# Kernel tuning notes

Measured on AMD Instinct MI355X. Metric: run time of the kernel, lower is better.

The kernel has to match this reference:

```python
import jax, jax.numpy as jnp
import numpy as np

B, S, D, H = 4, 2048, 1024, 16
HD = D // H


def setup_inputs() -> dict:
    key = jax.random.key(0)
    ks = jax.random.split(key, 9)
    s = 1.0 / np.sqrt(D)
    return {
        "x": jax.random.normal(ks[0], (B, S, D), dtype=jnp.float32),
        "Wq": jax.random.normal(ks[1], (D, D), dtype=jnp.float32) * s,
        "bq": jnp.zeros((D,), dtype=jnp.float32),
        "Wk": jax.random.normal(ks[2], (D, D), dtype=jnp.float32) * s,
        "bk": jnp.zeros((D,), dtype=jnp.float32),
        "Wv": jax.random.normal(ks[3], (D, D), dtype=jnp.float32) * s,
        "bv": jnp.zeros((D,), dtype=jnp.float32),
        "Wo": jax.random.normal(ks[4], (D, D), dtype=jnp.float32) * s,
        "bo": jnp.zeros((D,), dtype=jnp.float32),
    }


def reference(x, Wq, bq, Wk, bk, Wv, bv, Wo, bo):
    b, s, d = x.shape
    # project and split heads -> [b, h, s, hd]
    def split_heads(t):
        return t.reshape(b, s, H, HD).transpose(0, 2, 1, 3)
    q = split_heads(x @ Wq.T + bq)
    k = split_heads(x @ Wk.T + bk)
    v = split_heads(x @ Wv.T + bv)
    scale = 1.0 / np.sqrt(HD).astype(np.float32)
    att = jnp.einsum('bhqd,bhkd->bhqk', q, k) * scale
    causal = jnp.tril(jnp.ones((s, s), dtype=bool))
    att = jnp.where(causal[None, None], att, -jnp.inf)
    att = jax.nn.softmax(att, axis=-1)
    out = jnp.einsum('bhqk,bhkd->bhqd', att, v)  # [b,h,s,hd]
    out = out.transpose(0, 2, 1, 3).reshape(b, s, d)
    return out @ Wo.T + bo
```

## Files before the change

### kernel.cpp

```cpp
#include <hip/hip_runtime.h>
#include <hip/hip_bf16.h>
#include <math.h>

typedef __hip_bfloat16 bf16;
typedef __attribute__((ext_vector_type(8))) __bf16 bf16x8;
typedef __attribute__((ext_vector_type(4))) float f32x4;

__device__ __forceinline__ void gload_lds16(const void* g, void* l) {
  __builtin_amdgcn_global_load_lds(
      (const __attribute__((address_space(1))) unsigned int*)g,
      (__attribute__((address_space(3))) unsigned int*)l, 16, 0, 0);
}

__global__ void cvt_bf16(const float* __restrict__ in, bf16* __restrict__ out, int n) {
  int idx = (blockIdx.x * blockDim.x + threadIdx.x) * 8;
  if (idx >= n) return;
  float4 v0 = *(const float4*)(in + idx);
  float4 v1 = *(const float4*)(in + idx + 4);
  alignas(16) bf16 tmp[8];
  tmp[0] = __float2bfloat16(v0.x); tmp[1] = __float2bfloat16(v0.y);
  tmp[2] = __float2bfloat16(v0.z); tmp[3] = __float2bfloat16(v0.w);
  tmp[4] = __float2bfloat16(v1.x); tmp[5] = __float2bfloat16(v1.y);
  tmp[6] = __float2bfloat16(v1.z); tmp[7] = __float2bfloat16(v1.w);
  *(uint4*)(out + idx) = *(const uint4*)tmp;
}

__global__ void prep_w(const float* __restrict__ Wq, const float* __restrict__ Wk,
                       const float* __restrict__ Wv, const float* __restrict__ Wo,
                       const float* __restrict__ bq, const float* __restrict__ bk,
                       const float* __restrict__ bv,
                       bf16* __restrict__ wqkv, bf16* __restrict__ wo16,
                       float* __restrict__ b3) {
  const int bi = blockIdx.x;
  if (bi < 2048) {
    const int seg = bi >> 9;
    const int idx = ((bi & 511) * 256 + threadIdx.x) * 8;
    const float* src = seg == 0 ? Wq : seg == 1 ? Wk : seg == 2 ? Wv : Wo;
    bf16* dst = seg < 3 ? wqkv + (size_t)seg * 1048576 : wo16;
    float4 v0 = *(const float4*)(src + idx);
    float4 v1 = *(const float4*)(src + idx + 4);
    alignas(16) bf16 tmp[8];
    tmp[0] = __float2bfloat16(v0.x); tmp[1] = __float2bfloat16(v0.y);
    tmp[2] = __float2bfloat16(v0.z); tmp[3] = __float2bfloat16(v0.w);
    tmp[4] = __float2bfloat16(v1.x); tmp[5] = __float2bfloat16(v1.y);
    tmp[6] = __float2bfloat16(v1.z); tmp[7] = __float2bfloat16(v1.w);
    *(uint4*)(dst + idx) = *(const uint4*)tmp;
  } else {
    const int i = (bi - 2048) * 256 + threadIdx.x;
    if (i < 3072) b3[i] = i < 1024 ? bq[i] : i < 2048 ? bk[i - 1024] : bv[i - 2048];
  }
}

template<int MODE>
__global__ __launch_bounds__(512, 2) void gemm3(
    const bf16* __restrict__ A, const bf16* __restrict__ Bw,
    const float* __restrict__ bias, void* __restrict__ Cout,
    bf16* __restrict__ vt, int N, int K)
{
  constexpr int SLOT = 24576;
  __shared__ bf16 lds[3 * SLOT];
  const int tid = threadIdx.x;
  const int wave = tid >> 6, lane = tid & 63;
  const int lhi = lane >> 4, llo = lane & 15;
  const int wr = wave >> 2, wc = wave & 3;

  const int nbn = N >> 8;
  int wg = blockIdx.x;
  wg = (wg & 7) * (gridDim.x >> 3) + (wg >> 3);
  const int row0 = (wg / nbn) * 128, col0 = (wg % nbn) * 256;

  auto stageA = [&](int t) {
    bf16* s = &lds[(t % 3) * SLOT];
    const size_t k0 = (size_t)t << 6;
#pragma unroll
    for (int j = 0; j < 2; ++j) {
      int i = j * 512 + tid;
      int r = i >> 3, gl = (i & 7) ^ (r & 7);
      gload_lds16(A + (size_t)(row0 + r) * K + k0 + gl * 8, s + i * 8);
    }
  };
  auto stageBh = [&](int t, int half) {
    bf16* s = &lds[(t % 3) * SLOT] + 8192;
    const size_t k0 = (size_t)t << 6;
#pragma unroll
    for (int j = 0; j < 2; ++j) {
      int i = half * 1024 + j * 512 + tid;
      int r = i >> 3, gl = (i & 7) ^ (r & 7);
      gload_lds16(Bw + (size_t)(col0 + r) * K + k0 + gl * 8, s + i * 8);
    }
  };

  f32x4 acc[4][4] = {};
  const int T = K >> 6;

  stageA(0); stageBh(0, 0); stageBh(0, 1);
  stageA(1); stageBh(1, 0); stageBh(1, 1);
  asm volatile("s_waitcnt vmcnt(6)" ::: "memory");
  __builtin_amdgcn_s_barrier();

  for (int t = 0; t < T; ++t) {
    const bf16* sa = &lds[(t % 3) * SLOT];
    const bf16* sb = sa + 8192;

    bf16x8 af[4][2], bfr[2][2];
#pragma unroll
    for (int m = 0; m < 4; ++m)
#pragma unroll
      for (int kk = 0; kk < 2; ++kk) {
        int r = wr * 64 + m * 16 + llo;
        af[m][kk] = *(const bf16x8*)&sa[r * 64 + (((kk * 4 + lhi) ^ (r & 7)) << 3)];
      }
#pragma unroll
    for (int n = 0; n < 2; ++n)
#pragma unroll
      for (int kk = 0; kk < 2; ++kk) {
        int c = wc * 64 + n * 16 + llo;
        bfr[n][kk] = *(const bf16x8*)&sb[c * 64 + (((kk * 4 + lhi) ^ (c & 7)) << 3)];
      }
    if (t + 2 < T) { stageA(t + 2); stageBh(t + 2, 0); }
    __builtin_amdgcn_s_barrier();
    __builtin_amdgcn_s_setprio(1);
#pragma unroll
    for (int m = 0; m < 4; ++m)
#pragma unroll
      for (int n = 0; n < 2; ++n)
#pragma unroll
        for (int kk = 0; kk < 2; ++kk)
          acc[m][n] = __builtin_amdgcn_mfma_f32_16x16x32_bf16(af[m][kk], bfr[n][kk], acc[m][n], 0, 0, 0);
    __builtin_amdgcn_s_setprio(0);
    __builtin_amdgcn_s_barrier();

#pragma unroll
    for (int n = 0; n < 2; ++n)
#pragma unroll
      for (int kk = 0; kk < 2; ++kk) {
        int c = wc * 64 + 32 + n * 16 + llo;
        bfr[n][kk] = *(const bf16x8*)&sb[c * 64 + (((kk * 4 + lhi) ^ (c & 7)) << 3)];
      }
    if (t + 2 < T) stageBh(t + 2, 1);
    __builtin_amdgcn_s_barrier();
    __builtin_amdgcn_s_setprio(1);
#pragma unroll
    for (int m = 0; m < 4; ++m)
#pragma unroll
      for (int n = 0; n < 2; ++n)
#pragma unroll
        for (int kk = 0; kk < 2; ++kk)
          acc[m][2 + n] = __builtin_amdgcn_mfma_f32_16x16x32_bf16(af[m][kk], bfr[n][kk], acc[m][2 + n], 0, 0, 0);
    __builtin_amdgcn_s_setprio(0);
    if (t + 2 < T)      asm volatile("s_waitcnt vmcnt(6)" ::: "memory");
    else if (t + 1 < T) asm volatile("s_waitcnt vmcnt(0)" ::: "memory");
    __builtin_amdgcn_s_barrier();
  }

#pragma unroll
  for (int m = 0; m < 4; ++m)
#pragma unroll
    for (int n = 0; n < 4; ++n) {
      const int col = col0 + wc * 64 + (n & 1) * 16 + (n >> 1) * 32 + llo;
      const float bv = bias[col];
      const int rowbase = row0 + wr * 64 + m * 16 + lhi * 4;
      if (MODE == 1) {
#pragma unroll
        for (int j = 0; j < 4; ++j)
          ((float*)Cout)[(size_t)(rowbase + j) * N + col] = acc[m][n][j] + bv;
      } else if (col < 2048) {
#pragma unroll
        for (int j = 0; j < 4; ++j)
          ((bf16*)Cout)[(size_t)(rowbase + j) * N + col] = __float2bfloat16(acc[m][n][j] + bv);
      } else {
        const int hh = (col - 2048) >> 6, d = (col - 2048) & 63;
        const int bb = rowbase >> 11, s0 = rowbase & 2047;
        alignas(8) bf16 tmp[4];
#pragma unroll
        for (int j = 0; j < 4; ++j) tmp[j] = __float2bfloat16(acc[m][n][j] + bv);
        *(uint2*)&vt[((size_t)(bb * 16 + hh) * 64 + d) * 2048 + s0] = *(const uint2*)tmp;
      }
    }
}

__global__ __launch_bounds__(256, 2) void attn(
    const bf16* __restrict__ QKV, const bf16* __restrict__ Vt,
    bf16* __restrict__ O)
{
  const int S = 2048, DM = 3072;
  const int qpair = blockIdx.x, h = blockIdx.y, b = blockIdx.z;
  const int tid = threadIdx.x, wave = tid >> 6, lane = tid & 63;
  const int lhi = lane >> 4, llo = lane & 15;

  __shared__ bf16 lK[2][64 * 64];
  __shared__ bf16 lV[2][64 * 64];
  __shared__ bf16 lP[4][2][16 * 64];

  const size_t rowb = (size_t)b * S;
  const float scl = 0.125f * 1.4426950408889634f;

  bf16x8 vones;
#pragma unroll
  for (int i = 0; i < 8; ++i) vones[i] = (__bf16)1.0f;

  for (int job = 0; job < 2; ++job) {
    const int qt = job ? (15 - qpair) : qpair;
    const int q0 = qt * 128;
    const int nkt = 2 * qt + 2;

    auto stageKV = [&](int buf, int kt) {
#pragma unroll
      for (int it = 0; it < 2; ++it) {
        int i = it * 256 + tid;
        int r = i >> 3;
        int ce = ((i & 7) * 8) ^ ((r & 7) << 3);
        gload_lds16(&QKV[(rowb + (size_t)kt * 64 + r) * DM + 1024 + h * 64 + ce],
                    &lK[buf][i * 8]);
        gload_lds16(&Vt[((size_t)(b * 16 + h) * 64 + r) * S + kt * 64 + ce],
                    &lV[buf][i * 8]);
      }
    };

    bf16x8 qf[2][2];
#pragma unroll
    for (int hh = 0; hh < 2; ++hh)
#pragma unroll
      for (int kk = 0; kk < 2; ++kk)
        qf[hh][kk] = *(const bf16x8*)&QKV[(rowb + q0 + wave * 32 + hh * 16 + llo) * DM
                                          + h * 64 + kk * 32 + lhi * 8];

    f32x4 o_acc[2][4] = {};
    f32x4 o_l[2] = {};
    float m_run[2] = { -INFINITY, -INFINITY };

    __syncthreads();
    stageKV(0, 0);
    for (int kt = 0; kt < nkt; ++kt) {
      __syncthreads();
      if (kt + 1 < nkt) stageKV((kt + 1) & 1, kt + 1);
      const int buf = kt & 1;

      f32x4 s[2][4] = {};
#pragma unroll
      for (int kk = 0; kk < 2; ++kk)
#pragma unroll
        for (int n = 0; n < 4; ++n) {
          const int kr = n * 16 + llo;
          bf16x8 kf = *(const bf16x8*)&lK[buf][kr * 64 + ((kk * 32 + lhi * 8) ^ ((kr & 7) << 3))];
#pragma unroll
          for (int hh = 0; hh < 2; ++hh)
            s[hh][n] = __builtin_amdgcn_mfma_f32_16x16x32_bf16(kf, qf[hh][kk], s[hh][n], 0, 0, 0);
        }

      if (kt >= nkt - 2) {
#pragma unroll
        for (int hh = 0; hh < 2; ++hh) {
          const int lim = q0 + wave * 32 + hh * 16 + llo - kt * 64;
#pragma unroll
          for (int n = 0; n < 4; ++n)
#pragma unroll
            for (int j = 0; j < 4; ++j)
              if (n * 16 + lhi * 4 + j > lim) s[hh][n][j] = -INFINITY;
        }
      }

#pragma unroll
      for (int hh = 0; hh < 2; ++hh) {
        float m1 = fmaxf(fmaxf(s[hh][0][0], s[hh][0][1]), s[hh][0][2]);
        float m2 = fmaxf(fmaxf(s[hh][0][3], s[hh][1][0]), s[hh][1][1]);
        float m3 = fmaxf(fmaxf(s[hh][1][2], s[hh][1][3]), s[hh][2][0]);
        float m4 = fmaxf(fmaxf(s[hh][2][1], s[hh][2][2]), s[hh][2][3]);
        float m5 = fmaxf(fmaxf(s[hh][3][0], s[hh][3][1]), s[hh][3][2]);
        float mx = fmaxf(fmaxf(fmaxf(m1, m2), fmaxf(m3, m4)), fmaxf(m5, s[hh][3][3]));
        mx = fmaxf(mx, __shfl_xor(mx, 16));
        mx = fmaxf(mx, __shfl_xor(mx, 32));

        if (__any((mx - m_run[hh]) * scl > 8.0f)) {
          const float mnew = fmaxf(m_run[hh], mx);
          const float corr = exp2f((m_run[hh] - mnew) * scl);
          o_l[hh] *= corr;
#pragma unroll
          for (int n = 0; n < 4; ++n)
#pragma unroll
            for (int j = 0; j < 4; ++j) o_acc[hh][n][j] *= corr;
          m_run[hh] = mnew;
        }

        const float ms = m_run[hh] * scl;
#pragma unroll
        for (int n = 0; n < 4; ++n)
#pragma unroll
          for (int j = 0; j < 4; ++j)
            s[hh][n][j] = exp2f(fmaf(s[hh][n][j], scl, -ms));

#pragma unroll
        for (int n = 0; n < 4; ++n) {
          alignas(8) bf16 tmp[4];
#pragma unroll
          for (int j = 0; j < 4; ++j) tmp[j] = __float2bfloat16(s[hh][n][j]);
          const int g = (n * 4 + lhi) ^ ((llo & 7) << 1);
          *(uint2*)&lP[wave][hh][llo * 64 + g * 4] = *(const uint2*)tmp;
        }
      }

#pragma unroll
      for (int kk = 0; kk < 2; ++kk) {
        const int g0 = (kk * 8 + lhi * 2) ^ ((llo & 7) << 1);
        bf16x8 pf[2];
#pragma unroll
        for (int hh = 0; hh < 2; ++hh)
          pf[hh] = *(const bf16x8*)&lP[wave][hh][llo * 64 + g0 * 4];
#pragma unroll
        for (int n = 0; n < 4; ++n) {
          const int vr = n * 16 + llo;
          bf16x8 vf = *(const bf16x8*)&lV[buf][vr * 64 + ((kk * 32 + lhi * 8) ^ ((vr & 7) << 3))];
#pragma unroll
          for (int hh = 0; hh < 2; ++hh)
            o_acc[hh][n] = __builtin_amdgcn_mfma_f32_16x16x32_bf16(vf, pf[hh], o_acc[hh][n], 0, 0, 0);
        }
#pragma unroll
        for (int hh = 0; hh < 2; ++hh)
          o_l[hh] = __builtin_amdgcn_mfma_f32_16x16x32_bf16(vones, pf[hh], o_l[hh], 0, 0, 0);
      }
    }

#pragma unroll
    for (int hh = 0; hh < 2; ++hh) {
      const float inv = 1.0f / o_l[hh][0];
      const size_t orow = (rowb + q0 + wave * 32 + hh * 16 + llo) * 1024 + h * 64;
#pragma unroll
      for (int n = 0; n < 4; ++n) {
        alignas(8) bf16 tmp[4];
#pragma unroll
        for (int j = 0; j < 4; ++j) tmp[j] = __float2bfloat16(o_acc[hh][n][j] * inv);
        *(uint2*)&O[orow + n * 16 + lhi * 4] = *(const uint2*)tmp;
      }
    }
  }
}

extern "C" void kernel_launch(void* const* d_in, const int* in_sizes, int n_in,
                              void* d_out, int out_size, void* d_ws, size_t ws_size,
                              hipStream_t stream) {
  const float* x  = (const float*)d_in[0];
  const float* Wq = (const float*)d_in[1];
  const float* bq = (const float*)d_in[2];
  const float* Wk = (const float*)d_in[3];
  const float* bk = (const float*)d_in[4];
  const float* Wv = (const float*)d_in[5];
  const float* bv = (const float*)d_in[6];
  const float* Wo = (const float*)d_in[7];
  const float* bo = (const float*)d_in[8];

  const int Bb = 4, S = 2048, D = 1024;
  const int M = Bb * S;
  const int N3 = 3 * D;

  bf16* x16  = (bf16*)d_ws;
  bf16* wqkv = x16 + (size_t)M * D;
  bf16* wo16 = wqkv + (size_t)3 * D * D;
  bf16* qkv  = wo16 + (size_t)D * D;
  bf16* vt   = qkv + (size_t)M * N3;
  float* b3  = (float*)(vt + (size_t)M * D);
  size_t needed = ((size_t)M * D * 3 + 4 * (size_t)D * D + (size_t)M * N3) * 2 + 3072 * 4;
  if (ws_size < needed) return;

  cvt_bf16<<<(M * D) / (8 * 256), 256, 0, stream>>>(x, x16, M * D);
  prep_w<<<2060, 256, 0, stream>>>(Wq, Wk, Wv, Wo, bq, bk, bv, wqkv, wo16, b3);

  gemm3<0><<<(M / 128) * (N3 / 256), 512, 0, stream>>>(x16, wqkv, b3, qkv, vt, N3, D);
  attn<<<dim3(8, 16, Bb), 256, 0, stream>>>(qkv, vt, x16);
  gemm3<1><<<(M / 128) * (D / 256), 512, 0, stream>>>(x16, wo16, bo, d_out, nullptr, D, D);
}
```

Measured before the change: 200.1 us.

## Split attention work across eight waves with one 16-row Q tile each

The attention kernel now launches 512 threads (8 waves) per block instead of 256. Each wave handles 16 query rows instead of two 16-row sub-tiles, so per-wave register state (accumulators, scores, Q fragments) is halved. K/V staging now takes one load per thread. The aim is more waves in flight to hide latency and higher occupancy, at the cost of less reuse of each K/V LDS fragment read per MFMA and more LDS read traffic.

```diff
diff --git a/kernel.cpp b/kernel.cpp
--- a/kernel.cpp
+++ b/kernel.cpp
@@ -179,7 +179,7 @@
     }
 }
 
-__global__ __launch_bounds__(256, 2) void attn(
+__global__ __launch_bounds__(512, 4) void attn(
     const bf16* __restrict__ QKV, const bf16* __restrict__ Vt,
     bf16* __restrict__ O)
 {
@@ -190,7 +190,7 @@
 
   __shared__ bf16 lK[2][64 * 64];
   __shared__ bf16 lV[2][64 * 64];
-  __shared__ bf16 lP[4][2][16 * 64];
+  __shared__ bf16 lP[8][16 * 64];
 
   const size_t rowb = (size_t)b * S;
   const float scl = 0.125f * 1.4426950408889634f;
@@ -205,29 +205,23 @@
     const int nkt = 2 * qt + 2;
 
     auto stageKV = [&](int buf, int kt) {
-#pragma unroll
-      for (int it = 0; it < 2; ++it) {
-        int i = it * 256 + tid;
-        int r = i >> 3;
-        int ce = ((i & 7) * 8) ^ ((r & 7) << 3);
-        gload_lds16(&QKV[(rowb + (size_t)kt * 64 + r) * DM + 1024 + h * 64 + ce],
-                    &lK[buf][i * 8]);
-        gload_lds16(&Vt[((size_t)(b * 16 + h) * 64 + r) * S + kt * 64 + ce],
-                    &lV[buf][i * 8]);
-      }
+      const int i = tid;
+      const int r = i >> 3;
+      const int ce = ((i & 7) * 8) ^ ((r & 7) << 3);
+      gload_lds16(&QKV[(rowb + (size_t)kt * 64 + r) * DM + 1024 + h * 64 + ce],
+                  &lK[buf][i * 8]);
+      gload_lds16(&Vt[((size_t)(b * 16 + h) * 64 + r) * S + kt * 64 + ce],
+                  &lV[buf][i * 8]);
     };
 
-    bf16x8 qf[2][2];
-#pragma unroll
-    for (int hh = 0; hh < 2; ++hh)
-#pragma unroll
-      for (int kk = 0; kk < 2; ++kk)
-        qf[hh][kk] = *(const bf16x8*)&QKV[(rowb + q0 + wave * 32 + hh * 16 + llo) * DM
-                                          + h * 64 + kk * 32 + lhi * 8];
-
-    f32x4 o_acc[2][4] = {};
-    f32x4 o_l[2] = {};
-    float m_run[2] = { -INFINITY, -INFINITY };
+    bf16x8 qf[2];
+#pragma unroll
+    for (int kk = 0; kk < 2; ++kk)
+      qf[kk] = *(const bf16x8*)&QKV[(rowb + q0 + wave * 16 + llo) * DM + h * 64 + kk * 32 + lhi * 8];
+
+    f32x4 o_acc[4] = {};
+    f32x4 o_l = {};
+    float m_run = -INFINITY;
 
     __syncthreads();
     stageKV(0, 0);
@@ -236,101 +230,83 @@
       if (kt + 1 < nkt) stageKV((kt + 1) & 1, kt + 1);
       const int buf = kt & 1;
 
-      f32x4 s[2][4] = {};
+      f32x4 s[4] = {};
 #pragma unroll
       for (int kk = 0; kk < 2; ++kk)
 #pragma unroll
         for (int n = 0; n < 4; ++n) {
           const int kr = n * 16 + llo;
           bf16x8 kf = *(const bf16x8*)&lK[buf][kr * 64 + ((kk * 32 + lhi * 8) ^ ((kr & 7) << 3))];
-#pragma unroll
-          for (int hh = 0; hh < 2; ++hh)
-            s[hh][n] = __builtin_amdgcn_mfma_f32_16x16x32_bf16(kf, qf[hh][kk], s[hh][n], 0, 0, 0);
+          s[n] = __builtin_amdgcn_mfma_f32_16x16x32_bf16(kf, qf[kk], s[n], 0, 0, 0);
         }
 
       if (kt >= nkt - 2) {
-#pragma unroll
-        for (int hh = 0; hh < 2; ++hh) {
-          const int lim = q0 + wave * 32 + hh * 16 + llo - kt * 64;
-#pragma unroll
-          for (int n = 0; n < 4; ++n)
-#pragma unroll
-            for (int j = 0; j < 4; ++j)
-              if (n * 16 + lhi * 4 + j > lim) s[hh][n][j] = -INFINITY;
-        }
-      }
-
-#pragma unroll
-      for (int hh = 0; hh < 2; ++hh) {
-        float m1 = fmaxf(fmaxf(s[hh][0][0], s[hh][0][1]), s[hh][0][2]);
-        float m2 = fmaxf(fmaxf(s[hh][0][3], s[hh][1][0]), s[hh][1][1]);
-        float m3 = fmaxf(fmaxf(s[hh][1][2], s[hh][1][3]), s[hh][2][0]);
-        float m4 = fmaxf(fmaxf(s[hh][2][1], s[hh][2][2]), s[hh][2][3]);
-        float m5 = fmaxf(fmaxf(s[hh][3][0], s[hh][3][1]), s[hh][3][2]);
-        float mx = fmaxf(fmaxf(fmaxf(m1, m2), fmaxf(m3, m4)), fmaxf(m5, s[hh][3][3]));
-        mx = fmaxf(mx, __shfl_xor(mx, 16));
-        mx = fmaxf(mx, __shfl_xor(mx, 32));
-
-        if (__any((mx - m_run[hh]) * scl > 8.0f)) {
-          const float mnew = fmaxf(m_run[hh], mx);
-          const float corr = exp2f((m_run[hh] - mnew) * scl);
-          o_l[hh] *= corr;
-#pragma unroll
-          for (int n = 0; n < 4; ++n)
-#pragma unroll
-            for (int j = 0; j < 4; ++j) o_acc[hh][n][j] *= corr;
-          m_run[hh] = mnew;
-        }
-
-        const float ms = m_run[hh] * scl;
+        const int lim = q0 + wave * 16 + llo - kt * 64;
 #pragma unroll
         for (int n = 0; n < 4; ++n)
 #pragma unroll
           for (int j = 0; j < 4; ++j)
-            s[hh][n][j] = exp2f(fmaf(s[hh][n][j], scl, -ms));
-
-#pragma unroll
-        for (int n = 0; n < 4; ++n) {
-          alignas(8) bf16 tmp[4];
-#pragma unroll
-          for (int j = 0; j < 4; ++j) tmp[j] = __float2bfloat16(s[hh][n][j]);
-          const int g = (n * 4 + lhi) ^ ((llo & 7) << 1);
-          *(uint2*)&lP[wave][hh][llo * 64 + g * 4] = *(const uint2*)tmp;
-        }
+            if (n * 16 + lhi * 4 + j > lim) s[n][j] = -INFINITY;
+      }
+
+      float m1 = fmaxf(fmaxf(s[0][0], s[0][1]), s[0][2]);
+      float m2 = fmaxf(fmaxf(s[0][3], s[1][0]), s[1][1]);
+      float m3 = fmaxf(fmaxf(s[1][2], s[1][3]), s[2][0]);
+      float m4 = fmaxf(fmaxf(s[2][1], s[2][2]), s[2][3]);
+      float m5 = fmaxf(fmaxf(s[3][0], s[3][1]), s[3][2]);
+      float mx = fmaxf(fmaxf(fmaxf(m1, m2), fmaxf(m3, m4)), fmaxf(m5, s[3][3]));
+      mx = fmaxf(mx, __shfl_xor(mx, 16));
+      mx = fmaxf(mx, __shfl_xor(mx, 32));
+
+      if (__any((mx - m_run) * scl > 8.0f)) {
+        const float mnew = fmaxf(m_run, mx);
+        const float corr = exp2f((m_run - mnew) * scl);
+        o_l *= corr;
+#pragma unroll
+        for (int n = 0; n < 4; ++n)
+#pragma unroll
+          for (int j = 0; j < 4; ++j) o_acc[n][j] *= corr;
+        m_run = mnew;
+      }
+
+      const float ms = m_run * scl;
+#pragma unroll
+      for (int n = 0; n < 4; ++n)
+#pragma unroll
+        for (int j = 0; j < 4; ++j)
+          s[n][j] = exp2f(fmaf(s[n][j], scl, -ms));
+
+#pragma unroll
+      for (int n = 0; n < 4; ++n) {
+        alignas(8) bf16 tmp[4];
+#pragma unroll
+        for (int j = 0; j < 4; ++j) tmp[j] = __float2bfloat16(s[n][j]);
+        const int g = (n * 4 + lhi) ^ ((llo & 7) << 1);
+        *(uint2*)&lP[wave][llo * 64 + g * 4] = *(const uint2*)tmp;
       }
 
 #pragma unroll
       for (int kk = 0; kk < 2; ++kk) {
         const int g0 = (kk * 8 + lhi * 2) ^ ((llo & 7) << 1);
-        bf16x8 pf[2];
-#pragma unroll
-        for (int hh = 0; hh < 2; ++hh)
-          pf[hh] = *(const bf16x8*)&lP[wave][hh][llo * 64 + g0 * 4];
+        bf16x8 pf = *(const bf16x8*)&lP[wave][llo * 64 + g0 * 4];
 #pragma unroll
         for (int n = 0; n < 4; ++n) {
           const int vr = n * 16 + llo;
           bf16x8 vf = *(const bf16x8*)&lV[buf][vr * 64 + ((kk * 32 + lhi * 8) ^ ((vr & 7) << 3))];
-#pragma unroll
-          for (int hh = 0; hh < 2; ++hh)
-            o_acc[hh][n] = __builtin_amdgcn_mfma_f32_16x16x32_bf16(vf, pf[hh], o_acc[hh][n], 0, 0, 0);
+          o_acc[n] = __builtin_amdgcn_mfma_f32_16x16x32_bf16(vf, pf, o_acc[n], 0, 0, 0);
         }
-#pragma unroll
-        for (int hh = 0; hh < 2; ++hh)
-          o_l[hh] = __builtin_amdgcn_mfma_f32_16x16x32_bf16(vones, pf[hh], o_l[hh], 0, 0, 0);
-      }
-    }
-
-#pragma unroll
-    for (int hh = 0; hh < 2; ++hh) {
-      const float inv = 1.0f / o_l[hh][0];
-      const size_t orow = (rowb + q0 + wave * 32 + hh * 16 + llo) * 1024 + h * 64;
-#pragma unroll
-      for (int n = 0; n < 4; ++n) {
-        alignas(8) bf16 tmp[4];
-#pragma unroll
-        for (int j = 0; j < 4; ++j) tmp[j] = __float2bfloat16(o_acc[hh][n][j] * inv);
-        *(uint2*)&O[orow + n * 16 + lhi * 4] = *(const uint2*)tmp;
-      }
+        o_l = __builtin_amdgcn_mfma_f32_16x16x32_bf16(vones, pf, o_l, 0, 0, 0);
+      }
+    }
+
+    const float inv = 1.0f / o_l[0];
+    const size_t orow = (rowb + q0 + wave * 16 + llo) * 1024 + h * 64;
+#pragma unroll
+    for (int n = 0; n < 4; ++n) {
+      alignas(8) bf16 tmp[4];
+#pragma unroll
+      for (int j = 0; j < 4; ++j) tmp[j] = __float2bfloat16(o_acc[n][j] * inv);
+      *(uint2*)&O[orow + n * 16 + lhi * 4] = *(const uint2*)tmp;
     }
   }
 }
@@ -365,6 +341,6 @@
   prep_w<<<2060, 256, 0, stream>>>(Wq, Wk, Wv, Wo, bq, bk, bv, wqkv, wo16, b3);
 
   gemm3<0><<<(M / 128) * (N3 / 256), 512, 0, stream>>>(x16, wqkv, b3, qkv, vt, N3, D);
-  attn<<<dim3(8, 16, Bb), 256, 0, stream>>>(qkv, vt, x16);
+  attn<<<dim3(8, 16, Bb), 512, 0, stream>>>(qkv, vt, x16);
   gemm3<1><<<(M / 128) * (D / 256), 512, 0, stream>>>(x16, wo16, bo, d_out, nullptr, D, D);
 }
```

New measurement: 191.9 us. 1.04x faster.
